# Kernel tuning notes

Measured on AMD Instinct MI355X. Metric: run time of the kernel, lower is better.

The kernel has to match this reference:

```python
import jax, jax.numpy as jnp
import numpy as np

NU, NI = 100000, 100000   # num users / items
DU, DI = 128, 128         # input feature dims
H, O = 256, 256           # hidden_channels, out_channels
ER, EA = 500000, 500000   # edges: reviews, also_bought


def setup_inputs() -> dict:
    key = jax.random.key(0)
    ks = jax.random.split(key, 30)

    def W(k, i, o):
        return jax.random.normal(k, (i, o), jnp.float32) * np.float32(1.0 / np.sqrt(i))

    return {
        "x_user": jax.random.normal(ks[0], (NU, DU), jnp.float32),
        "x_item": jax.random.normal(ks[1], (NI, DI), jnp.float32),
        "src_rev": jax.random.randint(ks[2], (ER,), 0, NU, jnp.int32),
        "dst_rev": jax.random.randint(ks[3], (ER,), 0, NI, jnp.int32),
        "src_ab": jax.random.randint(ks[4], (EA,), 0, NI, jnp.int32),
        "dst_ab": jax.random.randint(ks[5], (EA,), 0, NI, jnp.int32),
        # layer 1 (SAGEConv per edge type): lin_l (neighbor), lin_r (root), bias on lin_l
        "Wl1_rev": W(ks[6], DU, H), "Wr1_rev": W(ks[7], DI, H), "b1_rev": jnp.zeros((H,), jnp.float32),
        "Wl1_rrev": W(ks[8], DI, H), "Wr1_rrev": W(ks[9], DU, H), "b1_rrev": jnp.zeros((H,), jnp.float32),
        "Wl1_ab": W(ks[10], DI, H), "Wr1_ab": W(ks[11], DI, H), "b1_ab": jnp.zeros((H,), jnp.float32),
        # layer 2
        "Wl2_rev": W(ks[12], H, O), "Wr2_rev": W(ks[13], H, O), "b2_rev": jnp.zeros((O,), jnp.float32),
        "Wl2_rrev": W(ks[14], H, O), "Wr2_rrev": W(ks[15], H, O), "b2_rrev": jnp.zeros((O,), jnp.float32),
        "Wl2_ab": W(ks[16], H, O), "Wr2_ab": W(ks[17], H, O), "b2_ab": jnp.zeros((O,), jnp.float32),
    }


def sage_conv(x_src, x_dst, src, dst, Wl, b, Wr):
    """PyG SAGEConv: lin_l(mean of neighbor feats) + lin_r(x_dst); mean of empty set = 0."""
    n_dst = x_dst.shape[0]
    msg_sum = jax.ops.segment_sum(x_src[src], dst, num_segments=n_dst)   # [n_dst, d_src]
    cnt = jax.ops.segment_sum(jnp.ones(dst.shape, x_src.dtype), dst, num_segments=n_dst)
    mean = msg_sum / jnp.maximum(cnt, 1.0)[:, None]
    return mean @ Wl + b + x_dst @ Wr


def reference(x_user, x_item, src_rev, dst_rev, src_ab, dst_ab,
              Wl1_rev, Wr1_rev, b1_rev, Wl1_rrev, Wr1_rrev, b1_rrev, Wl1_ab, Wr1_ab, b1_ab,
              Wl2_rev, Wr2_rev, b2_rev, Wl2_rrev, Wr2_rrev, b2_rrev, Wl2_ab, Wr2_ab, b2_ab):
    # layer 1 + HeteroConv sum aggregation across edge types per dst node type
    h_item = (sage_conv(x_user, x_item, src_rev, dst_rev, Wl1_rev, b1_rev, Wr1_rev)
              + sage_conv(x_item, x_item, src_ab, dst_ab, Wl1_ab, b1_ab, Wr1_ab))
    # rev_reviews = transpose of reviews: item -> user
    h_user = sage_conv(x_item, x_user, dst_rev, src_rev, Wl1_rrev, b1_rrev, Wr1_rrev)
    h_item = jax.nn.relu(h_item)
    h_user = jax.nn.relu(h_user)
    # layer 2
    o_item = (sage_conv(h_user, h_item, src_rev, dst_rev, Wl2_rev, b2_rev, Wr2_rev)
              + sage_conv(h_item, h_item, src_ab, dst_ab, Wl2_ab, b2_ab, Wr2_ab))
    o_user = sage_conv(h_item, h_user, dst_rev, src_rev, Wl2_rrev, b2_rrev, Wr2_rrev)
    return (o_user, o_item)
```

## Files before the change

kernel.cpp:

```cpp
#include <hip/hip_runtime.h>
#include <hip/hip_bf16.h>

#define NN    100000
#define MPAD  100096
#define ER_   500000
#define EA_   500000
#define NCH   25
#define F_RELU 2

typedef __attribute__((ext_vector_type(8))) _Float16 f16x8;
typedef __attribute__((ext_vector_type(4))) float f32x4;
typedef __attribute__((address_space(3))) uint lds_uint;
typedef const __attribute__((address_space(1))) uint g_uint;

union H8 { uint4 u; _Float16 h[8]; };
union H1 { _Float16 h; ushort u; };

__device__ __forceinline__ ushort f2h(float f) { H1 c; c.h = (_Float16)f; return c.u; }

__global__ void count3(const int* __restrict__ dst_rev, const int* __restrict__ dst_ab,
                       const int* __restrict__ src_rev, int* __restrict__ cnt ) {
    int i = blockIdx.x * blockDim.x + threadIdx.x;
    if (i < ER_)                 atomicAdd(&cnt[dst_rev[i]], 1);
    else if (i < ER_ + EA_)      atomicAdd(&cnt[NN + dst_ab[i - ER_]], 1);
    else if (i < ER_ + EA_ + ER_) atomicAdd(&cnt[2 * NN + src_rev[i - ER_ - EA_]], 1);
}

__global__ void fill3(const int* __restrict__ dst_rev, const int* __restrict__ src_rev,
                      const int* __restrict__ dst_ab, const int* __restrict__ src_ab,
                      const int* __restrict__ pA, const int* __restrict__ pB,
                      const int* __restrict__ pC, int* __restrict__ cur ,
                      int* __restrict__ colA, int* __restrict__ colB, int* __restrict__ colC) {
    int i = blockIdx.x * blockDim.x + threadIdx.x;
    if (i < ER_) {
        int d = dst_rev[i];
        colA[pA[d] + atomicAdd(&cur[d], 1)] = src_rev[i];
    } else if (i < ER_ + EA_) {
        int e = i - ER_, d = dst_ab[e];
        colB[pB[d] + atomicAdd(&cur[NN + d], 1)] = src_ab[e];
    } else if (i < ER_ + EA_ + ER_) {
        int e = i - ER_ - EA_, d = src_rev[e];
        colC[pC[d] + atomicAdd(&cur[2 * NN + d], 1)] = dst_rev[e];
    }
}

__global__ void scan_part(const int* __restrict__ cnt , int* __restrict__ part) {
    int b = blockIdx.x, a = b / NCH, c = b % NCH;
    const int* src = cnt + a * NN;
    int base = c * 4096 + threadIdx.x * 16;
    int s = 0;
    #pragma unroll
    for (int k = 0; k < 16; k += 4) {
        int i = base + k;
        if (i + 3 < NN) { int4 v = *(const int4*)(src + i); s += v.x + v.y + v.z + v.w; }
        else { for (int j = 0; j < 4; j++) if (i + j < NN) s += src[i + j]; }
    }
    __shared__ int ws[4];
    int lane = threadIdx.x & 63, wid = threadIdx.x >> 6;
    #pragma unroll
    for (int o = 32; o > 0; o >>= 1) s += __shfl_down(s, o, 64);
    if (lane == 0) ws[wid] = s;
    __syncthreads();
    if (threadIdx.x == 0) part[b] = ws[0] + ws[1] + ws[2] + ws[3];
}

__global__ void scan_off(const int* __restrict__ part, int* __restrict__ choff,
                         int* __restrict__ pA, int* __restrict__ pB, int* __restrict__ pC) {
    int a = threadIdx.x;
    if (a < 3) {
        int acc = 0;
        for (int c = 0; c < NCH; c++) { choff[a * NCH + c] = acc; acc += part[a * NCH + c]; }
        int* p = (a == 0) ? pA : (a == 1) ? pB : pC;
        p[NN] = acc;
    }
}

__global__ void scan_apply(const int* __restrict__ cnt, const int* __restrict__ choff,
                           int* __restrict__ pA, int* __restrict__ pB, int* __restrict__ pC) {
    int b = blockIdx.x, a = b / NCH, c = b % NCH;
    const int* src = cnt + a * NN;
    int* ptr = (a == 0) ? pA : (a == 1) ? pB : pC;
    int tid = threadIdx.x, lane = tid & 63, wid = tid >> 6;
    int base = c * 4096 + tid * 16;
    int v[16], s = 0;
    #pragma unroll
    for (int k = 0; k < 16; k++) { int i = base + k; v[k] = (i < NN) ? src[i] : 0; s += v[k]; }
    int isc = s;
    #pragma unroll
    for (int o = 1; o < 64; o <<= 1) { int t = __shfl_up(isc, o, 64); if (lane >= o) isc += t; }
    __shared__ int wsum[4];
    if (lane == 63) wsum[wid] = isc;
    __syncthreads();
    int woff = 0;
    for (int wj = 0; wj < wid; wj++) woff += wsum[wj];
    int excl = choff[a * NCH + c] + woff + (isc - s);
    #pragma unroll
    for (int k = 0; k < 16; k++) { int i = base + k; if (i < NN) ptr[i] = excl; excl += v[k]; }
}

struct PrepArgs {
    const float* xsrc[2]; ushort* xdst[2];
    const float* W0[10]; const float* W1[10]; ushort* T[10];
};

__global__ void prep_all(PrepArgs A) {
    const long CVB = (long)MPAD * 128 / 8 / 256;
    long b = blockIdx.x;
    if (b < 2 * CVB) {
        int which = (b >= CVB);
        long lb = b - which * CVB;
        long i = (lb * 256 + threadIdx.x) * 8;
        const float* x = A.xsrc[which];
        ushort* o = A.xdst[which];
        float4 v0 = {0.f,0.f,0.f,0.f}, v1 = {0.f,0.f,0.f,0.f};
        if (i < (long)NN * 128) { v0 = *(const float4*)(x + i); v1 = *(const float4*)(x + i + 4); }
        H8 r;
        r.h[0]=(_Float16)v0.x; r.h[1]=(_Float16)v0.y; r.h[2]=(_Float16)v0.z; r.h[3]=(_Float16)v0.w;
        r.h[4]=(_Float16)v1.x; r.h[5]=(_Float16)v1.y; r.h[6]=(_Float16)v1.z; r.h[7]=(_Float16)v1.w;
        *(uint4*)(o + i) = r.u;
        return;
    }
    long j = (b - 2 * CVB) * 256 + threadIdx.x;
    int idx, rem, K;
    if (j < 5 * 32768) { idx = j >> 15; rem = j & 32767; K = 128; }
    else {
        long j2 = j - 5 * 32768;
        if (j2 >= 5L * 65536) return;
        idx = 5 + (int)(j2 >> 16); rem = (int)(j2 & 65535); K = 256;
    }
    int k = rem >> 8, n = rem & 255;
    float v = A.W0[idx][rem];
    if (A.W1[idx]) v += A.W1[idx][rem];
    A.T[idx][n * K + k] = f2h(v);
}

__global__ void agg3_128(const ushort* __restrict__ xu, const ushort* __restrict__ xi,
                         const int* __restrict__ pA, const int* __restrict__ cA,
                         const int* __restrict__ pB, const int* __restrict__ cB,
                         const int* __restrict__ pC, const int* __restrict__ cC,
                         ushort* __restrict__ sA, ushort* __restrict__ sB,
                         ushort* __restrict__ sC) {
    const int SEG = MPAD * 8 / 256;
    int seg = blockIdx.x / SEG, lb = blockIdx.x % SEG;
    int dir = seg % 3, half = seg / 3;
    const ushort* x; const int* ptr; const int* col; ushort* out;
    if (dir == 0)      { x = xu; ptr = pA; col = cA; out = sA; }
    else if (dir == 1) { x = xi; ptr = pB; col = cB; out = sB; }
    else               { x = xi; ptr = pC; col = cC; out = sC; }
    int g = lb * 256 + threadIdx.x;
    int node = g >> 3, l = g & 7;
    if (node >= MPAD) return;
    int doff = half * 64 + l * 8;
    size_t ob = (size_t)node * 128 + doff;
    if (node >= NN) { *(uint4*)(out + ob) = make_uint4(0,0,0,0); return; }
    const ushort* xb = x + doff;
    int p0 = ptr[node], p1 = ptr[node + 1];
    float a[8] = {0.f,0.f,0.f,0.f,0.f,0.f,0.f,0.f};
    int e = p0;
    for (; e + 4 <= p1; e += 4) {
        int c0 = col[e], c1 = col[e+1], c2 = col[e+2], c3 = col[e+3];
        H8 v0, v1, v2, v3;
        v0.u = *(const uint4*)(xb + (size_t)c0 * 128);
        v1.u = *(const uint4*)(xb + (size_t)c1 * 128);
        v2.u = *(const uint4*)(xb + (size_t)c2 * 128);
        v3.u = *(const uint4*)(xb + (size_t)c3 * 128);
        #pragma unroll
        for (int k = 0; k < 8; k++) a[k] += (float)v0.h[k];
        #pragma unroll
        for (int k = 0; k < 8; k++) a[k] += (float)v1.h[k];
        #pragma unroll
        for (int k = 0; k < 8; k++) a[k] += (float)v2.h[k];
        #pragma unroll
        for (int k = 0; k < 8; k++) a[k] += (float)v3.h[k];
    }
    for (; e < p1; ++e) {
        H8 v; v.u = *(const uint4*)(xb + (size_t)col[e] * 128);
        #pragma unroll
        for (int k = 0; k < 8; k++) a[k] += (float)v.h[k];
    }
    float inv = (p1 > p0) ? 1.0f / (float)(p1 - p0) : 0.0f;
    H8 r;
    #pragma unroll
    for (int k = 0; k < 8; k++) r.h[k] = (_Float16)(a[k] * inv);
    *(uint4*)(out + ob) = r.u;
}

__global__ void agg3_256(const ushort* __restrict__ hU, const ushort* __restrict__ hI,
                         const int* __restrict__ pA, const int* __restrict__ cA,
                         const int* __restrict__ pB, const int* __restrict__ cB,
                         const int* __restrict__ pC, const int* __restrict__ cC,
                         ushort* __restrict__ sA, ushort* __restrict__ sB,
                         ushort* __restrict__ sC) {
    const int SEG = MPAD * 16 / 256;
    int seg = blockIdx.x / SEG, lb = blockIdx.x % SEG;
    int dir = seg % 3, half = seg / 3;
    const ushort* x; const int* ptr; const int* col; ushort* out;
    if (dir == 0)      { x = hU; ptr = pA; col = cA; out = sA; }
    else if (dir == 1) { x = hI; ptr = pB; col = cB; out = sB; }
    else               { x = hI; ptr = pC; col = cC; out = sC; }
    int g = lb * 256 + threadIdx.x;
    int node = g >> 4, l = g & 15;
    if (node >= MPAD) return;
    int doff = half * 128 + l * 8;
    size_t ob = (size_t)node * 256 + doff;
    if (node >= NN) { *(uint4*)(out + ob) = make_uint4(0,0,0,0); return; }
    const ushort* xb = x + doff;
    int p0 = ptr[node], p1 = ptr[node + 1];
    float a[8] = {0.f,0.f,0.f,0.f,0.f,0.f,0.f,0.f};
    int e = p0;
    for (; e + 4 <= p1; e += 4) {
        int c0 = col[e], c1 = col[e+1], c2 = col[e+2], c3 = col[e+3];
        H8 v0, v1, v2, v3;
        v0.u = *(const uint4*)(xb + (size_t)c0 * 256);
        v1.u = *(const uint4*)(xb + (size_t)c1 * 256);
        v2.u = *(const uint4*)(xb + (size_t)c2 * 256);
        v3.u = *(const uint4*)(xb + (size_t)c3 * 256);
        #pragma unroll
        for (int k = 0; k < 8; k++) a[k] += (float)v0.h[k];
        #pragma unroll
        for (int k = 0; k < 8; k++) a[k] += (float)v1.h[k];
        #pragma unroll
        for (int k = 0; k < 8; k++) a[k] += (float)v2.h[k];
        #pragma unroll
        for (int k = 0; k < 8; k++) a[k] += (float)v3.h[k];
    }
    for (; e < p1; ++e) {
        H8 v; v.u = *(const uint4*)(xb + (size_t)col[e] * 256);
        #pragma unroll
        for (int k = 0; k < 8; k++) a[k] += (float)v.h[k];
    }
    float inv = (p1 > p0) ? 1.0f / (float)(p1 - p0) : 0.0f;
    H8 r;
    #pragma unroll
    for (int k = 0; k < 8; k++) r.h[k] = (_Float16)(a[k] * inv);
    *(uint4*)(out + ob) = r.u;
}

struct GP {
    const ushort *A0, *W0, *A1, *W1, *A2, *W2;
    int ksh0, ksh1, ksh2;
    int c1, c2, S;
};

__global__ __launch_bounds__(256)
void gemm2x(GP Pa, const float* b0a, const float* b1a, float* Cfa, ushort* Cha, int fla,
            GP Pb, const float* b0b, const float* b1b, float* Cfb, ushort* Chb, int flb) {
    GP P; const float *b0, *b1; float* Cf; ushort* Ch; int flags;
    if (blockIdx.z == 0) { P = Pa; b0 = b0a; b1 = b1a; Cf = Cfa; Ch = Cha; flags = fla; }
    else                 { P = Pb; b0 = b0b; b1 = b1b; Cf = Cfb; Ch = Chb; flags = flb; }

    __shared__ ushort sA[2][128 * 64];
    __shared__ ushort sW[2][128 * 64];
    const int tid = threadIdx.x;
    const int m0 = blockIdx.x * 128, n0 = blockIdx.y * 128;
    const int lane = tid & 63, w = tid >> 6;
    const int wr = (w >> 1) * 64, wc = (w & 1) * 64;
    const int fcol = lane & 15, fq = lane >> 4;
    const int srow = tid >> 3, sc = tid & 7;

    f32x4 acc[4][4];
    #pragma unroll
    for (int i = 0; i < 4; i++)
        #pragma unroll
        for (int j = 0; j < 4; j++) acc[i][j] = (f32x4){0.f,0.f,0.f,0.f};

    auto stage = [&](int t, int buf) {
        if (t >= P.S) return;
        int p = (t >= P.c1) + (t >= P.c2);
        const ushort* A = (p == 2) ? P.A2 : (p == 1) ? P.A1 : P.A0;
        const ushort* W = (p == 2) ? P.W2 : (p == 1) ? P.W1 : P.W0;
        int ksh  = (p == 2) ? P.ksh2 : (p == 1) ? P.ksh1 : P.ksh0;
        int base = (p == 2) ? P.c2 : (p == 1) ? P.c1 : 0;
        int k0 = (t - base) << 6;
        #pragma unroll
        for (int ii = 0; ii < 4; ++ii) {
            int row = ii * 32 + srow;
            int q = sc ^ (row & 7);
            const ushort* srcA = A + (((size_t)(m0 + row)) << ksh) + k0 + q * 8;
            const ushort* srcW = W + (((size_t)(n0 + row)) << ksh) + k0 + q * 8;
            __builtin_amdgcn_global_load_lds((g_uint*)srcA,
                (lds_uint*)(&sA[buf][row * 64 + sc * 8]), 16, 0, 0);
            __builtin_amdgcn_global_load_lds((g_uint*)srcW,
                (lds_uint*)(&sW[buf][row * 64 + sc * 8]), 16, 0, 0);
        }
    };

    stage(0, 0);
    int cur = 0;
    #pragma unroll 1
    for (int t = 0; t < P.S; ++t) {
        __syncthreads();
        stage(t + 1, cur ^ 1);
        const ushort* bA = sA[cur];
        const ushort* bW = sW[cur];
        #pragma unroll
        for (int kk = 0; kk < 2; ++kk) {
            f16x8 a[4], b[4];
            #pragma unroll
            for (int i = 0; i < 4; ++i) {
                int ra = wr + i * 16 + fcol;
                int s = (fq + kk * 4) ^ (ra & 7);
                a[i] = *(const f16x8*)(bA + ra * 64 + s * 8);
            }
            #pragma unroll
            for (int j = 0; j < 4; ++j) {
                int rw = wc + j * 16 + fcol;
                int s = (fq + kk * 4) ^ (rw & 7);
                b[j] = *(const f16x8*)(bW + rw * 64 + s * 8);
            }
            #pragma unroll
            for (int i = 0; i < 4; ++i)
                #pragma unroll
                for (int j = 0; j < 4; ++j)
                    acc[i][j] = __builtin_amdgcn_mfma_f32_16x16x32_f16(a[i], b[j], acc[i][j], 0, 0, 0);
        }
        cur ^= 1;
    }

    const bool relu = flags & F_RELU;
    float bb[4];
    #pragma unroll
    for (int j = 0; j < 4; ++j) {
        int cg = n0 + wc + j * 16 + fcol;
        float v = 0.f;
        if (b0) v += b0[cg];
        if (b1) v += b1[cg];
        bb[j] = v;
    }
    #pragma unroll
    for (int i = 0; i < 4; ++i) {
        #pragma unroll
        for (int r = 0; r < 4; ++r) {
            int gm = m0 + wr + i * 16 + fq * 4 + r;
            if (gm >= NN) continue;
            size_t rowb = (size_t)gm * 256;
            #pragma unroll
            for (int j = 0; j < 4; ++j) {
                size_t idx = rowb + n0 + wc + j * 16 + fcol;
                float v = acc[i][j][r] + bb[j];
                if (relu) v = fmaxf(v, 0.f);
                if (Ch) Ch[idx] = f2h(v);
                else    Cf[idx] = v;
            }
        }
    }
}

extern "C" void kernel_launch(void* const* d_in, const int* in_sizes, int n_in,
                              void* d_out, int out_size, void* d_ws, size_t ws_size,
                              hipStream_t stream) {
    const float* x_user = (const float*)d_in[0];
    const float* x_item = (const float*)d_in[1];
    const int* src_rev  = (const int*)d_in[2];
    const int* dst_rev  = (const int*)d_in[3];
    const int* src_ab   = (const int*)d_in[4];
    const int* dst_ab   = (const int*)d_in[5];
    const float* Wl1_rev  = (const float*)d_in[6];
    const float* Wr1_rev  = (const float*)d_in[7];
    const float* b1_rev   = (const float*)d_in[8];
    const float* Wl1_rrev = (const float*)d_in[9];
    const float* Wr1_rrev = (const float*)d_in[10];
    const float* b1_rrev  = (const float*)d_in[11];
    const float* Wl1_ab   = (const float*)d_in[12];
    const float* Wr1_ab   = (const float*)d_in[13];
    const float* b1_ab    = (const float*)d_in[14];
    const float* Wl2_rev  = (const float*)d_in[15];
    const float* Wr2_rev  = (const float*)d_in[16];
    const float* b2_rev   = (const float*)d_in[17];
    const float* Wl2_rrev = (const float*)d_in[18];
    const float* Wr2_rrev = (const float*)d_in[19];
    const float* b2_rrev  = (const float*)d_in[20];
    const float* Wl2_ab   = (const float*)d_in[21];
    const float* Wr2_ab   = (const float*)d_in[22];
    const float* b2_ab    = (const float*)d_in[23];

    float* o_user = (float*)d_out;
    float* o_item = (float*)d_out + (size_t)NN * 256;

    char* ws = (char*)d_ws;
    size_t off = 0;
    auto alloc = [&](size_t bytes) -> void* {
        void* p = ws + off;
        off += (bytes + 255) & ~(size_t)255;
        return p;
    };
    const size_t P256 = (size_t)MPAD * 256 * 2;
    const size_t P128 = (size_t)MPAD * 128 * 2;
    ushort* xu     = (ushort*)alloc(P128);
    ushort* xi     = (ushort*)alloc(P128);
    ushort* slabA  = (ushort*)alloc(P128);
    ushort* slabB  = (ushort*)alloc(P128);
    ushort* slabC  = (ushort*)alloc(P128);
    ushort* hI     = (ushort*)alloc(P256);
    ushort* hU     = (ushort*)alloc(P256);
    ushort* s2A    = (ushort*)alloc(P256);
    ushort* s2B    = (ushort*)alloc(P256);
    ushort* s2C    = (ushort*)alloc(P256);
    const size_t W1SZ = 128 * 256 * 2, W2SZ = 256 * 256 * 2;
    ushort* wt_l1rev  = (ushort*)alloc(W1SZ);
    ushort* wt_l1ab   = (ushort*)alloc(W1SZ);
    ushort* wt_l1rrev = (ushort*)alloc(W1SZ);
    ushort* wt_r1c    = (ushort*)alloc(W1SZ);
    ushort* wt_r1rrev = (ushort*)alloc(W1SZ);
    ushort* wt_l2rev  = (ushort*)alloc(W2SZ);
    ushort* wt_l2ab   = (ushort*)alloc(W2SZ);
    ushort* wt_l2rrev = (ushort*)alloc(W2SZ);
    ushort* wt_r2c    = (ushort*)alloc(W2SZ);
    ushort* wt_r2rrev = (ushort*)alloc(W2SZ);
    int* ptrA = (int*)alloc((NN + 1) * 4);
    int* ptrB = (int*)alloc((NN + 1) * 4);
    int* ptrC = (int*)alloc((NN + 1) * 4);
    int* colA = (int*)alloc((size_t)ER_ * 4);
    int* colB = (int*)alloc((size_t)EA_ * 4);
    int* colC = (int*)alloc((size_t)ER_ * 4);
    int* cnt3 = (int*)alloc((size_t)3 * NN * 4);
    int* part  = (int*)alloc(3 * NCH * 4);
    int* choff = (int*)alloc(3 * NCH * 4);

    const int TPB = 256;
    const int NE3 = ER_ + EA_ + ER_;
    dim3 e3grid((NE3 + TPB - 1) / TPB);

    hipMemsetAsync(cnt3, 0, (size_t)3 * NN * 4, stream);
    count3<<<e3grid, TPB, 0, stream>>>(dst_rev, dst_ab, src_rev, cnt3);
    scan_part<<<3 * NCH, TPB, 0, stream>>>(cnt3, part);
    scan_off<<<1, 64, 0, stream>>>(part, choff, ptrA, ptrB, ptrC);
    scan_apply<<<3 * NCH, TPB, 0, stream>>>(cnt3, choff, ptrA, ptrB, ptrC);
    hipMemsetAsync(cnt3, 0, (size_t)3 * NN * 4, stream);
    fill3<<<e3grid, TPB, 0, stream>>>(dst_rev, src_rev, dst_ab, src_ab,
                                      ptrA, ptrB, ptrC, cnt3, colA, colB, colC);

    PrepArgs PA;
    PA.xsrc[0] = x_user; PA.xdst[0] = xu;
    PA.xsrc[1] = x_item; PA.xdst[1] = xi;
    const float* W0s[10] = {Wl1_rev, Wl1_ab, Wl1_rrev, Wr1_rev, Wr1_rrev,
                            Wl2_rev, Wl2_ab, Wl2_rrev, Wr2_rev, Wr2_rrev};
    const float* W1s[10] = {nullptr, nullptr, nullptr, Wr1_ab, nullptr,
                            nullptr, nullptr, nullptr, Wr2_ab, nullptr};
    ushort* Ts[10] = {wt_l1rev, wt_l1ab, wt_l1rrev, wt_r1c, wt_r1rrev,
                      wt_l2rev, wt_l2ab, wt_l2rrev, wt_r2c, wt_r2rrev};
    for (int i = 0; i < 10; i++) { PA.W0[i] = W0s[i]; PA.W1[i] = W1s[i]; PA.T[i] = Ts[i]; }
    const long CVB = (long)MPAD * 128 / 8 / 256;
    const long WPB = (5 * 32768 + 5 * 65536 + 255) / 256;
    prep_all<<<(int)(2 * CVB + WPB), TPB, 0, stream>>>(PA);

    dim3 ggrid(MPAD / 128, 2, 2);

    auto mkGP = [&](const ushort* a0, const ushort* w0, int K0,
                    const ushort* a1, const ushort* w1, int K1,
                    const ushort* a2, const ushort* w2, int K2) {
        GP P;
        P.A0 = a0; P.W0 = w0;
        P.A1 = a1 ? a1 : a0; P.W1 = w1 ? w1 : w0;
        P.A2 = a2 ? a2 : a0; P.W2 = w2 ? w2 : w0;
        P.ksh0 = (K0 == 256) ? 8 : 7;
        P.ksh1 = (K1 == 256) ? 8 : 7;
        P.ksh2 = (K2 == 256) ? 8 : 7;
        P.c1 = K0 >> 6; P.c2 = P.c1 + (K1 >> 6); P.S = P.c2 + (K2 >> 6);
        return P;
    };

    agg3_128<<<6 * (MPAD * 8 / 256), TPB, 0, stream>>>(xu, xi, ptrA, colA, ptrB, colB,
                                                       ptrC, colC, slabA, slabB, slabC);
    {
        GP P0 = mkGP(slabA, wt_l1rev, 128, slabB, wt_l1ab, 128, xi, wt_r1c, 128);
        GP P1 = mkGP(slabC, wt_l1rrev, 128, xu, wt_r1rrev, 128, nullptr, nullptr, 0);
        gemm2x<<<ggrid, TPB, 0, stream>>>(P0, b1_rev, b1_ab, nullptr, hI, F_RELU,
                                          P1, b1_rrev, nullptr, nullptr, hU, F_RELU);
    }

    agg3_256<<<6 * (MPAD * 16 / 256), TPB, 0, stream>>>(hU, hI, ptrA, colA, ptrB, colB,
                                                        ptrC, colC, s2A, s2B, s2C);
    {
        GP P0 = mkGP(s2A, wt_l2rev, 256, s2B, wt_l2ab, 256, hI, wt_r2c, 256);
        GP P1 = mkGP(s2C, wt_l2rrev, 256, hU, wt_r2rrev, 256, nullptr, nullptr, 0);
        gemm2x<<<ggrid, TPB, 0, stream>>>(P0, b2_rev, b2_ab, o_item, nullptr, 0,
                                          P1, b2_rrev, nullptr, o_user, nullptr, 0);
    }
}
```

Before: 911.5 us.

## Widen GEMM tile to full 256 output columns with 512 threads, single-buffered

The fused GEMM kernel now has each block cover all 256 output columns with 8 waves (512 threads), so each A tile is loaded from global memory once instead of twice across two column blocks. Double buffering is dropped in favour of a single LDS buffer with load, barrier, compute and barrier on every K step. This halves A-operand traffic and halves the block count, but global loads no longer overlap with MFMA work, and fewer, larger blocks may reduce occupancy.

```diff
diff --git a/kernel.cpp b/kernel.cpp
--- a/kernel.cpp
+++ b/kernel.cpp
@@ -242,19 +242,19 @@
     int c1, c2, S;
 };
 
-__global__ __launch_bounds__(256)
+__global__ __launch_bounds__(512)
 void gemm2x(GP Pa, const float* b0a, const float* b1a, float* Cfa, ushort* Cha, int fla,
             GP Pb, const float* b0b, const float* b1b, float* Cfb, ushort* Chb, int flb) {
     GP P; const float *b0, *b1; float* Cf; ushort* Ch; int flags;
     if (blockIdx.z == 0) { P = Pa; b0 = b0a; b1 = b1a; Cf = Cfa; Ch = Cha; flags = fla; }
     else                 { P = Pb; b0 = b0b; b1 = b1b; Cf = Cfb; Ch = Chb; flags = flb; }
 
-    __shared__ ushort sA[2][128 * 64];
-    __shared__ ushort sW[2][128 * 64];
+    __shared__ ushort sA[128 * 64];
+    __shared__ ushort sW[256 * 64];
     const int tid = threadIdx.x;
-    const int m0 = blockIdx.x * 128, n0 = blockIdx.y * 128;
+    const int m0 = blockIdx.x * 128;
     const int lane = tid & 63, w = tid >> 6;
-    const int wr = (w >> 1) * 64, wc = (w & 1) * 64;
+    const int wr = (w >> 2) * 64, wc = (w & 3) * 64;
     const int fcol = lane & 15, fq = lane >> 4;
     const int srow = tid >> 3, sc = tid & 7;
 
@@ -264,35 +264,33 @@
         #pragma unroll
         for (int j = 0; j < 4; j++) acc[i][j] = (f32x4){0.f,0.f,0.f,0.f};
 
-    auto stage = [&](int t, int buf) {
-        if (t >= P.S) return;
+    #pragma unroll 1
+    for (int t = 0; t < P.S; ++t) {
         int p = (t >= P.c1) + (t >= P.c2);
         const ushort* A = (p == 2) ? P.A2 : (p == 1) ? P.A1 : P.A0;
         const ushort* W = (p == 2) ? P.W2 : (p == 1) ? P.W1 : P.W0;
         int ksh  = (p == 2) ? P.ksh2 : (p == 1) ? P.ksh1 : P.ksh0;
         int base = (p == 2) ? P.c2 : (p == 1) ? P.c1 : 0;
         int k0 = (t - base) << 6;
-        #pragma unroll
-        for (int ii = 0; ii < 4; ++ii) {
-            int row = ii * 32 + srow;
+
+        #pragma unroll
+        for (int ii = 0; ii < 2; ++ii) {
+            int row = ii * 64 + srow;
             int q = sc ^ (row & 7);
             const ushort* srcA = A + (((size_t)(m0 + row)) << ksh) + k0 + q * 8;
-            const ushort* srcW = W + (((size_t)(n0 + row)) << ksh) + k0 + q * 8;
             __builtin_amdgcn_global_load_lds((g_uint*)srcA,
-                (lds_uint*)(&sA[buf][row * 64 + sc * 8]), 16, 0, 0);
+                (lds_uint*)(sA + row * 64 + sc * 8), 16, 0, 0);
+        }
+        #pragma unroll
+        for (int ii = 0; ii < 4; ++ii) {
+            int row = ii * 64 + srow;
+            int q = sc ^ (row & 7);
+            const ushort* srcW = W + (((size_t)row) << ksh) + k0 + q * 8;
             __builtin_amdgcn_global_load_lds((g_uint*)srcW,
-                (lds_uint*)(&sW[buf][row * 64 + sc * 8]), 16, 0, 0);
+                (lds_uint*)(sW + row * 64 + sc * 8), 16, 0, 0);
         }
-    };
-
-    stage(0, 0);
-    int cur = 0;
-    #pragma unroll 1
-    for (int t = 0; t < P.S; ++t) {
         __syncthreads();
-        stage(t + 1, cur ^ 1);
-        const ushort* bA = sA[cur];
-        const ushort* bW = sW[cur];
+
         #pragma unroll
         for (int kk = 0; kk < 2; ++kk) {
             f16x8 a[4], b[4];
@@ -300,13 +298,13 @@
             for (int i = 0; i < 4; ++i) {
                 int ra = wr + i * 16 + fcol;
                 int s = (fq + kk * 4) ^ (ra & 7);
-                a[i] = *(const f16x8*)(bA + ra * 64 + s * 8);
+                a[i] = *(const f16x8*)(sA + ra * 64 + s * 8);
             }
             #pragma unroll
             for (int j = 0; j < 4; ++j) {
                 int rw = wc + j * 16 + fcol;
                 int s = (fq + kk * 4) ^ (rw & 7);
-                b[j] = *(const f16x8*)(bW + rw * 64 + s * 8);
+                b[j] = *(const f16x8*)(sW + rw * 64 + s * 8);
             }
             #pragma unroll
             for (int i = 0; i < 4; ++i)
@@ -314,14 +312,14 @@
                 for (int j = 0; j < 4; ++j)
                     acc[i][j] = __builtin_amdgcn_mfma_f32_16x16x32_f16(a[i], b[j], acc[i][j], 0, 0, 0);
         }
-        cur ^= 1;
+        __syncthreads();
     }
 
     const bool relu = flags & F_RELU;
     float bb[4];
     #pragma unroll
     for (int j = 0; j < 4; ++j) {
-        int cg = n0 + wc + j * 16 + fcol;
+        int cg = wc + j * 16 + fcol;
         float v = 0.f;
         if (b0) v += b0[cg];
         if (b1) v += b1[cg];
@@ -336,7 +334,7 @@
             size_t rowb = (size_t)gm * 256;
             #pragma unroll
             for (int j = 0; j < 4; ++j) {
-                size_t idx = rowb + n0 + wc + j * 16 + fcol;
+                size_t idx = rowb + wc + j * 16 + fcol;
                 float v = acc[i][j][r] + bb[j];
                 if (relu) v = fmaxf(v, 0.f);
                 if (Ch) Ch[idx] = f2h(v);
@@ -444,7 +442,7 @@
     const long WPB = (5 * 32768 + 5 * 65536 + 255) / 256;
     prep_all<<<(int)(2 * CVB + WPB), TPB, 0, stream>>>(PA);
 
-    dim3 ggrid(MPAD / 128, 2, 2);
+    dim3 ggrid(MPAD / 128, 1, 2);
 
     auto mkGP = [&](const ushort* a0, const ushort* w0, int K0,
                     const ushort* a1, const ushort* w1, int K1,
@@ -465,7 +463,7 @@
     {
         GP P0 = mkGP(slabA, wt_l1rev, 128, slabB, wt_l1ab, 128, xi, wt_r1c, 128);
         GP P1 = mkGP(slabC, wt_l1rrev, 128, xu, wt_r1rrev, 128, nullptr, nullptr, 0);
-        gemm2x<<<ggrid, TPB, 0, stream>>>(P0, b1_rev, b1_ab, nullptr, hI, F_RELU,
+        gemm2x<<<ggrid, 512, 0, stream>>>(P0, b1_rev, b1_ab, nullptr, hI, F_RELU,
                                           P1, b1_rrev, nullptr, nullptr, hU, F_RELU);
     }
 
@@ -474,7 +472,7 @@
     {
         GP P0 = mkGP(s2A, wt_l2rev, 256, s2B, wt_l2ab, 256, hI, wt_r2c, 256);
         GP P1 = mkGP(s2C, wt_l2rrev, 256, hU, wt_r2rrev, 256, nullptr, nullptr, 0);
-        gemm2x<<<ggrid, TPB, 0, stream>>>(P0, b2_rev, b2_ab, o_item, nullptr, 0,
+        gemm2x<<<ggrid, 512, 0, stream>>>(P0, b2_rev, b2_ab, o_item, nullptr, 0,
                                           P1, b2_rrev, nullptr, o_user, nullptr, 0);
     }
 }
```

Result: faster. 816.8 us (-10.4%).
